# Kernel tuning notes

Measured on AMD Instinct MI355X. Metric: run time of the kernel, lower is better.

## Reference

```python
import jax, jax.numpy as jnp
import numpy as np
from jax import lax

B, T, D, H, O = 4096, 128, 128, 150, 10

def setup_inputs() -> dict:
    key = jax.random.key(0)
    k1, k2, k3 = jax.random.split(key, 3)
    X = jax.random.normal(k1, (B, T, D), dtype=jnp.float32)
    # BasicRNNCell kernel: acts on concat([x, h]) -> [D+H, H]
    W_cell = jax.random.normal(k2, (D + H, H), dtype=jnp.float32) * (1.0 / np.sqrt(D + H))
    b_cell = jnp.zeros((H,), dtype=jnp.float32)
    W_out = jax.random.normal(k3, (H, O), dtype=jnp.float32) * (1.0 / np.sqrt(H))
    b_out = jnp.zeros((O,), dtype=jnp.float32)
    return {"X": X, "W_cell": W_cell, "b_cell": b_cell, "W_out": W_out, "b_out": b_out}

def reference(X, W_cell, b_cell, W_out, b_out):
    # dynamic_rnn with BasicRNNCell: h_t = tanh([x_t, h_{t-1}] @ W + b)
    batch = X.shape[0]
    hid = W_cell.shape[1]
    xs = jnp.swapaxes(X, 0, 1)  # [T, B, D]
    h0 = jnp.zeros((batch, hid), dtype=X.dtype)

    def step(h, x_t):
        h_new = jnp.tanh(jnp.concatenate([x_t, h], axis=-1) @ W_cell + b_cell)
        return h_new, None

    h_final, _ = lax.scan(step, h0, xs)
    # dense classifier on final state (tf code applies dense to `states`)
    logits = h_final @ W_out + b_out  # [B, O]
    return logits
```

## Files before the change

kernel.cpp:

```cpp
#include <hip/hip_runtime.h>
#include <hip/hip_bf16.h>


typedef __bf16 bf16x8 __attribute__((ext_vector_type(8)));
typedef __bf16 bf16x4 __attribute__((ext_vector_type(4)));
typedef float  f32x4  __attribute__((ext_vector_type(4)));
typedef unsigned short u16;

#define B_  4096
#define T_  128
#define D_  128
#define H_  150
#define O_  10

#define KX 4
#define KH 5
#define HPAD 168
#define XPAD 136
#define ROWS 8

__global__ __launch_bounds__(256, 2) void rnn_fused(
    const float* __restrict__ X,
    const float* __restrict__ Wc,
    const float* __restrict__ bc,
    const float* __restrict__ Wo,
    const float* __restrict__ bo,
    float* __restrict__ out)
{
    __shared__ __attribute__((aligned(16))) __bf16 sh_h[2][ROWS][HPAD];
    __shared__ __attribute__((aligned(16))) __bf16 sh_x[3][ROWS][XPAD];

    const int tid  = threadIdx.x;
    const int wid  = tid >> 6;
    const int lane = tid & 63;
    const int q    = lane >> 4;
    const int l16  = lane & 15;
    const int arow = l16 & 7;
    const int row0 = blockIdx.x * ROWS;

    const int srow = tid >> 5;
    const int scol = (tid & 31) * 4;

    const int nt_cnt = (wid < 2) ? 3 : 2;
    const int tbase  = (wid < 2) ? wid * 3 : 6 + (wid - 2) * 2;
    const int cbase  = tbase * 16;

    {
        __bf16* p = &sh_h[0][0][0];
        for (int i = tid; i < 2 * ROWS * HPAD; i += 256) p[i] = (__bf16)0.f;
    }

    bf16x8 wx[3][KX];
    bf16x8 wh[3][KH];
    float  bias[3];
#pragma unroll
    for (int nt = 0; nt < 3; ++nt) {
        if (nt >= nt_cnt) break;
        const int  j   = (nt < 2) ? (cbase + 2 * l16 + nt) : (cbase + 32 + l16);
        const bool jv  = (j < H_);
        const int  jcl = jv ? j : 0;
        bias[nt] = jv ? bc[jcl] : 0.f;
#pragma unroll
        for (int kt = 0; kt < KX; ++kt) {
            bf16x8 f;
#pragma unroll
            for (int i = 0; i < 8; ++i) {
                const int k = kt * 32 + q * 8 + i;
                float v = Wc[k * H_ + jcl];
                v = fminf(fmaxf(v, -64.f), 64.f);
                f[i] = jv ? (__bf16)v : (__bf16)0.f;
            }
            wx[nt][kt] = f;
        }
#pragma unroll
        for (int kt = 0; kt < KH; ++kt) {
            bf16x8 f;
#pragma unroll
            for (int i = 0; i < 8; ++i) {
                const int  kh  = kt * 32 + q * 8 + i;
                const bool kv  = jv && (kh < H_);
                const int  khc = (kh < H_) ? kh : 0;
                float v = Wc[(D_ + khc) * H_ + jcl];
                v = fminf(fmaxf(v, -64.f), 64.f);
                f[i] = kv ? (__bf16)v : (__bf16)0.f;
            }
            wh[nt][kt] = f;
        }
    }

    const float* Xg = X + (size_t)(row0 + srow) * (T_ * D_) + scol;
#pragma unroll
    for (int s = 0; s < 2; ++s) {
        f32x4 v = *(const f32x4*)(Xg + (size_t)s * D_);
        bf16x4 w;
#pragma unroll
        for (int i = 0; i < 4; ++i) w[i] = (__bf16)v[i];
        *(bf16x4*)(&sh_x[s][srow][scol]) = w;
    }
    f32x4 xl_cur = *(const f32x4*)(Xg + (size_t)2 * D_);

    __syncthreads();

    int cur = 0;
    for (int t = 0; t < T_; ++t) {
        const int tt = (t + 3 < T_) ? (t + 3) : (T_ - 1);
        f32x4 xl_next = *(const f32x4*)(Xg + (size_t)tt * D_);

        const __bf16* xb = &sh_x[cur][0][0];
        const __bf16* hb = &sh_h[t & 1][0][0];
        bf16x8 a[KX], ah[KH];
#pragma unroll
        for (int kt = 0; kt < KX; ++kt)
            a[kt] = *(const bf16x8*)(xb + arow * XPAD + kt * 32 + q * 8);
#pragma unroll
        for (int kt = 0; kt < KH; ++kt)
            ah[kt] = *(const bf16x8*)(hb + arow * HPAD + kt * 32 + q * 8);

        f32x4 ax[3], ahh[3];
#pragma unroll
        for (int nt = 0; nt < 3; ++nt) {
            if (nt >= nt_cnt) break;
            ax[nt]  = (f32x4){bias[nt], bias[nt], bias[nt], bias[nt]};
            ahh[nt] = (f32x4){0.f, 0.f, 0.f, 0.f};
        }
#pragma unroll
        for (int kt = 0; kt < KX; ++kt) {
            ax[0] = __builtin_amdgcn_mfma_f32_16x16x32_bf16(a[kt], wx[0][kt], ax[0], 0, 0, 0);
            ax[1] = __builtin_amdgcn_mfma_f32_16x16x32_bf16(a[kt], wx[1][kt], ax[1], 0, 0, 0);
            if (nt_cnt == 3)
                ax[2] = __builtin_amdgcn_mfma_f32_16x16x32_bf16(a[kt], wx[2][kt], ax[2], 0, 0, 0);
        }
#pragma unroll
        for (int kt = 0; kt < KH; ++kt) {
            ahh[0] = __builtin_amdgcn_mfma_f32_16x16x32_bf16(ah[kt], wh[0][kt], ahh[0], 0, 0, 0);
            ahh[1] = __builtin_amdgcn_mfma_f32_16x16x32_bf16(ah[kt], wh[1][kt], ahh[1], 0, 0, 0);
            if (nt_cnt == 3)
                ahh[2] = __builtin_amdgcn_mfma_f32_16x16x32_bf16(ah[kt], wh[2][kt], ahh[2], 0, 0, 0);
        }

        {
            const int wslot = (cur == 0) ? 2 : cur - 1;
            bf16x4 w;
#pragma unroll
            for (int i = 0; i < 4; ++i) w[i] = (__bf16)xl_cur[i];
            *(bf16x4*)(&sh_x[wslot][srow][scol]) = w;
            xl_cur = xl_next;
        }

        __bf16 (*ho)[HPAD] = sh_h[(t + 1) & 1];
#pragma unroll
        for (int r = 0; r < 4; ++r) {
            const int rr = q * 4 + r;
            const float z0 = ax[0][r] + ahh[0][r];
            const float z1 = ax[1][r] + ahh[1][r];
            const float e0 = __builtin_amdgcn_exp2f(z0 * 2.8853900817779268f);
            const float e1 = __builtin_amdgcn_exp2f(z1 * 2.8853900817779268f);
            const float h0 = 1.f - 2.f * __builtin_amdgcn_rcpf(e0 + 1.f);
            const float h1 = 1.f - 2.f * __builtin_amdgcn_rcpf(e1 + 1.f);
            float h2 = 0.f;
            if (nt_cnt == 3) {
                const float z2 = ax[2][r] + ahh[2][r];
                const float e2 = __builtin_amdgcn_exp2f(z2 * 2.8853900817779268f);
                h2 = 1.f - 2.f * __builtin_amdgcn_rcpf(e2 + 1.f);
            }
            if (q < 2) {
                const unsigned p = (unsigned)__builtin_bit_cast(u16, (__bf16)h0)
                                 | ((unsigned)__builtin_bit_cast(u16, (__bf16)h1) << 16);
                *(unsigned*)(&ho[rr][cbase + 2 * l16]) = p;
                if (nt_cnt == 3)
                    ho[rr][cbase + 32 + l16] = (__bf16)h2;
            }
        }

        asm volatile("s_waitcnt lgkmcnt(0)\n\ts_barrier" ::: "memory");

        cur = (cur == 2) ? 0 : cur + 1;
    }

    __syncthreads();

    if (tid < ROWS * O_) {
        const int row = tid / O_;
        const int o   = tid - row * O_;
        float accv = bo[o];
        const __bf16* hf = &sh_h[0][row][0];
        for (int k = 0; k < H_; ++k)
            accv += (float)hf[k] * Wo[k * O_ + o];
        out[(size_t)(row0 + row) * O_ + o] = accv;
    }
}

extern "C" void kernel_launch(void* const* d_in, const int* in_sizes, int n_in,
                              void* d_out, int out_size, void* d_ws, size_t ws_size,
                              hipStream_t stream) {
    (void)in_sizes; (void)n_in; (void)out_size; (void)d_ws; (void)ws_size;
    const float* X  = (const float*)d_in[0];
    const float* Wc = (const float*)d_in[1];
    const float* bc = (const float*)d_in[2];
    const float* Wo = (const float*)d_in[3];
    const float* bo = (const float*)d_in[4];
    rnn_fused<<<dim3(B_ / ROWS), dim3(256), 0, stream>>>(X, Wc, bc, Wo, bo, (float*)d_out);
}
```

Measured before the change: 417.2 us.

## Use 16 rows per block with 8 waves splitting hidden column tiles

Doubles the batch rows per block to 16 so each MFMA 16x16 tile uses all 16 A rows instead of duplicating 8, and doubles the block to 512 threads (8 waves). Each wave now owns one or two 16-column output tiles instead of two or three, shortening the serial MFMA chain per timestep. This halves the grid size and uses larger blocks with fewer weight registers per wave, at the cost of more waves meeting at each per-step barrier.

```diff
diff --git a/kernel.cpp b/kernel.cpp
--- a/kernel.cpp
+++ b/kernel.cpp
@@ -17,9 +17,9 @@
 #define KH 5
 #define HPAD 168
 #define XPAD 136
-#define ROWS 8
+#define ROWS 16
 
-__global__ __launch_bounds__(256, 2) void rnn_fused(
+__global__ __launch_bounds__(512, 2) void rnn_fused(
     const float* __restrict__ X,
     const float* __restrict__ Wc,
     const float* __restrict__ bc,
@@ -35,28 +35,26 @@
     const int lane = tid & 63;
     const int q    = lane >> 4;
     const int l16  = lane & 15;
-    const int arow = l16 & 7;
     const int row0 = blockIdx.x * ROWS;
 
     const int srow = tid >> 5;
     const int scol = (tid & 31) * 4;
 
-    const int nt_cnt = (wid < 2) ? 3 : 2;
-    const int tbase  = (wid < 2) ? wid * 3 : 6 + (wid - 2) * 2;
-    const int cbase  = tbase * 16;
+    const int nt_cnt = (wid < 6) ? 1 : 2;
+    const int cbase  = (wid < 6) ? wid * 16 : ((wid == 6) ? 96 : 128);
 
     {
         __bf16* p = &sh_h[0][0][0];
-        for (int i = tid; i < 2 * ROWS * HPAD; i += 256) p[i] = (__bf16)0.f;
+        for (int i = tid; i < 2 * ROWS * HPAD; i += 512) p[i] = (__bf16)0.f;
     }
 
-    bf16x8 wx[3][KX];
-    bf16x8 wh[3][KH];
-    float  bias[3];
+    bf16x8 wx[2][KX];
+    bf16x8 wh[2][KH];
+    float  bias[2];
 #pragma unroll
-    for (int nt = 0; nt < 3; ++nt) {
+    for (int nt = 0; nt < 2; ++nt) {
         if (nt >= nt_cnt) break;
-        const int  j   = (nt < 2) ? (cbase + 2 * l16 + nt) : (cbase + 32 + l16);
+        const int  j   = (nt_cnt == 1) ? (cbase + l16) : (cbase + 2 * l16 + nt);
         const bool jv  = (j < H_);
         const int  jcl = jv ? j : 0;
         bias[nt] = jv ? bc[jcl] : 0.f;
@@ -111,31 +109,28 @@
         bf16x8 a[KX], ah[KH];
 #pragma unroll
         for (int kt = 0; kt < KX; ++kt)
-            a[kt] = *(const bf16x8*)(xb + arow * XPAD + kt * 32 + q * 8);
+            a[kt] = *(const bf16x8*)(xb + l16 * XPAD + kt * 32 + q * 8);
 #pragma unroll
         for (int kt = 0; kt < KH; ++kt)
-            ah[kt] = *(const bf16x8*)(hb + arow * HPAD + kt * 32 + q * 8);
+            ah[kt] = *(const bf16x8*)(hb + l16 * HPAD + kt * 32 + q * 8);
 
-        f32x4 ax[3], ahh[3];
+        f32x4 ax0 = (f32x4){bias[0], bias[0], bias[0], bias[0]};
+        f32x4 ah0 = (f32x4){0.f, 0.f, 0.f, 0.f};
+        f32x4 ax1 = (f32x4){bias[1], bias[1], bias[1], bias[1]};
+        f32x4 ah1 = (f32x4){0.f, 0.f, 0.f, 0.f};
 #pragma unroll
-        for (int nt = 0; nt < 3; ++nt) {
-            if (nt >= nt_cnt) break;
-            ax[nt]  = (f32x4){bias[nt], bias[nt], bias[nt], bias[nt]};
-            ahh[nt] = (f32x4){0.f, 0.f, 0.f, 0.f};
-        }
+        for (int kt = 0; kt < KX; ++kt)
+            ax0 = __builtin_amdgcn_mfma_f32_16x16x32_bf16(a[kt], wx[0][kt], ax0, 0, 0, 0);
 #pragma unroll
-        for (int kt = 0; kt < KX; ++kt) {
-            ax[0] = __builtin_amdgcn_mfma_f32_16x16x32_bf16(a[kt], wx[0][kt], ax[0], 0, 0, 0);
-            ax[1] = __builtin_amdgcn_mfma_f32_16x16x32_bf16(a[kt], wx[1][kt], ax[1], 0, 0, 0);
-            if (nt_cnt == 3)
-                ax[2] = __builtin_amdgcn_mfma_f32_16x16x32_bf16(a[kt], wx[2][kt], ax[2], 0, 0, 0);
-        }
+        for (int kt = 0; kt < KH; ++kt)
+            ah0 = __builtin_amdgcn_mfma_f32_16x16x32_bf16(ah[kt], wh[0][kt], ah0, 0, 0, 0);
+        if (nt_cnt == 2) {
 #pragma unroll
-        for (int kt = 0; kt < KH; ++kt) {
-            ahh[0] = __builtin_amdgcn_mfma_f32_16x16x32_bf16(ah[kt], wh[0][kt], ahh[0], 0, 0, 0);
-            ahh[1] = __builtin_amdgcn_mfma_f32_16x16x32_bf16(ah[kt], wh[1][kt], ahh[1], 0, 0, 0);
-            if (nt_cnt == 3)
-                ahh[2] = __builtin_amdgcn_mfma_f32_16x16x32_bf16(ah[kt], wh[2][kt], ahh[2], 0, 0, 0);
+            for (int kt = 0; kt < KX; ++kt)
+                ax1 = __builtin_amdgcn_mfma_f32_16x16x32_bf16(a[kt], wx[1][kt], ax1, 0, 0, 0);
+#pragma unroll
+            for (int kt = 0; kt < KH; ++kt)
+                ah1 = __builtin_amdgcn_mfma_f32_16x16x32_bf16(ah[kt], wh[1][kt], ah1, 0, 0, 0);
         }
 
         {
@@ -148,36 +143,33 @@
         }
 
         __bf16 (*ho)[HPAD] = sh_h[(t + 1) & 1];
+        if (nt_cnt == 1) {
 #pragma unroll
-        for (int r = 0; r < 4; ++r) {
-            const int rr = q * 4 + r;
-            const float z0 = ax[0][r] + ahh[0][r];
-            const float z1 = ax[1][r] + ahh[1][r];
-            const float e0 = __builtin_amdgcn_exp2f(z0 * 2.8853900817779268f);
-            const float e1 = __builtin_amdgcn_exp2f(z1 * 2.8853900817779268f);
-            const float h0 = 1.f - 2.f * __builtin_amdgcn_rcpf(e0 + 1.f);
-            const float h1 = 1.f - 2.f * __builtin_amdgcn_rcpf(e1 + 1.f);
-            float h2 = 0.f;
-            if (nt_cnt == 3) {
-                const float z2 = ax[2][r] + ahh[2][r];
-                const float e2 = __builtin_amdgcn_exp2f(z2 * 2.8853900817779268f);
-                h2 = 1.f - 2.f * __builtin_amdgcn_rcpf(e2 + 1.f);
+            for (int r = 0; r < 4; ++r) {
+                const float z0 = ax0[r] + ah0[r];
+                const float e0 = __builtin_amdgcn_exp2f(z0 * 2.8853900817779268f);
+                const float h0 = 1.f - 2.f * __builtin_amdgcn_rcpf(e0 + 1.f);
+                ho[q * 4 + r][cbase + l16] = (__bf16)h0;
             }
-            if (q < 2) {
+        } else {
+#pragma unroll
+            for (int r = 0; r < 4; ++r) {
+                const float z0 = ax0[r] + ah0[r];
+                const float z1 = ax1[r] + ah1[r];
+                const float e0 = __builtin_amdgcn_exp2f(z0 * 2.8853900817779268f);
+                const float e1 = __builtin_amdgcn_exp2f(z1 * 2.8853900817779268f);
+                const float h0 = 1.f - 2.f * __builtin_amdgcn_rcpf(e0 + 1.f);
+                const float h1 = 1.f - 2.f * __builtin_amdgcn_rcpf(e1 + 1.f);
                 const unsigned p = (unsigned)__builtin_bit_cast(u16, (__bf16)h0)
                                  | ((unsigned)__builtin_bit_cast(u16, (__bf16)h1) << 16);
-                *(unsigned*)(&ho[rr][cbase + 2 * l16]) = p;
-                if (nt_cnt == 3)
-                    ho[rr][cbase + 32 + l16] = (__bf16)h2;
+                *(unsigned*)(&ho[q * 4 + r][cbase + 2 * l16]) = p;
             }
         }
 
-        asm volatile("s_waitcnt lgkmcnt(0)\n\ts_barrier" ::: "memory");
+        __syncthreads();
 
         cur = (cur == 2) ? 0 : cur + 1;
     }
-
-    __syncthreads();
 
     if (tid < ROWS * O_) {
         const int row = tid / O_;
@@ -199,5 +191,5 @@
     const float* bc = (const float*)d_in[2];
     const float* Wo = (const float*)d_in[3];
     const float* bo = (const float*)d_in[4];
-    rnn_fused<<<dim3(B_ / ROWS), dim3(256), 0, stream>>>(X, Wc, bc, Wo, bo, (float*)d_out);
+    rnn_fused<<<dim3(B_ / ROWS), dim3(512), 0, stream>>>(X, Wc, bc, Wo, bo, (float*)d_out);
 }
```

New measurement: 393.5 us. 5.7% less time.
